# Optimization experiments

Hardware: AMD Instinct MI355X
Metric: run time of the kernel (lower is better)

The kernel has to match this reference:

```python
import jax, jax.numpy as jnp
import numpy as np

B = 4        # samples
GP = 6       # graphs per sample (K*2)
N = 1024     # nodes per graph
DIN = 128    # input feature dim
D = 128      # out_channels
E = 16384    # edges per graph


def setup_inputs() -> dict:
    k = jax.random.split(jax.random.key(0), 10)
    G = B * GP
    s = 0.05
    return {
        "x": jax.random.normal(k[0], (G, N, DIN), jnp.float32),
        "edge_attr": jax.random.uniform(k[1], (G, E, 6), jnp.float32),
        "gcn_W": jax.random.normal(k[2], (4, DIN, D), jnp.float32) * s,
        "gcn_b": jnp.zeros((4, D), jnp.float32),
        "Ws": jax.random.normal(k[3], (4, D, D), jnp.float32) * s,
        "lin1_W": jax.random.normal(k[4], (GP * D, 20), jnp.float32) * s,
        "lin1_b": jnp.zeros((20,), jnp.float32),
        "codefc_W": jax.random.normal(k[5], (20, 2), jnp.float32) * s,
        "codefc_b": jnp.zeros((2,), jnp.float32),
        "lin2_W": jax.random.normal(k[6], (GP * D, GP), jnp.float32) * s,
        "lin2_b": jnp.zeros((GP,), jnp.float32),
        "simfc_W": jax.random.normal(k[7], (GP, 2), jnp.float32) * s,
        "simfc_b": jnp.zeros((2,), jnp.float32),
        "edge_index": jax.random.randint(k[8], (G, 2, E), 0, N, jnp.int64),
    }


def _gcn(x, src, dst, ew, W, b):
    # PyG GCNConv with normalize=True, add_self_loops=True (self-loop weight 1)
    n = x.shape[0]
    deg = jax.ops.segment_sum(ew, dst, num_segments=n) + 1.0
    dinv = jax.lax.rsqrt(deg)
    xw = x @ W
    norm = dinv[src] * ew * dinv[dst]               # [E]
    agg = jax.ops.segment_sum(norm[:, None] * xw[src], dst, num_segments=n)
    return agg + (dinv * dinv)[:, None] * xw + b    # self-loop term + bias


def _gnnlayer(x, ei, ea, gcn_W, gcn_b, Ws):
    # x_tmp = sum_i relu(GCN_i(x, ew=edge_attr[:, i+2])) @ Ws[i]
    src, dst = ei[0], ei[1]
    def chan(W, b, Wmix, ew):
        return jnp.maximum(_gcn(x, src, dst, ew, W, b), 0.0) @ Wmix
    return jax.vmap(chan)(gcn_W, gcn_b, Ws, ea[:, 2:6].T).sum(0)  # [N, D]


def _forward(x, edge_attr, gcn_W, gcn_b, Ws, lin1_W, lin1_b, codefc_W,
             codefc_b, lin2_W, lin2_b, simfc_W, simfc_b, edge_index):
    # per-graph GNN layer over all G = B*GP graphs
    x_tmp = jax.vmap(lambda xg, eig, eag: _gnnlayer(xg, eig, eag, gcn_W, gcn_b, Ws))(
        x, edge_index, edge_attr)                    # [G, N, D]
    g = x_tmp.mean(axis=1).reshape(B, GP * D)        # g_matrix [B, 768]
    # L2-normalize rows (F.normalize eps=1e-12)
    xn = x_tmp / jnp.clip(jnp.linalg.norm(x_tmp, axis=-1, keepdims=True), 1e-12)
    xn = xn.reshape(B, GP, N, D)
    # all-pairs cosine sim -> tanh -> 21-bin histogram on [-1, 1] -> weighted sum
    S = jnp.tanh(jnp.einsum('bind,bjmd->bijnm', xn, xn))   # [B,GP,GP,N,N]
    idx = jnp.clip(jnp.floor((S + 1.0) * (21.0 / 2.0)).astype(jnp.int32), 0, 20)
    centers = jnp.linspace(-1.0, 1.0, 21, dtype=jnp.float32)
    # hist/(N*N) dot centers == mean of per-element bin centers
    sim = centers[idx].mean(axis=(3, 4))             # [B, GP, GP]
    # backnet
    feat = jnp.maximum(g @ lin1_W + lin1_b, 0.0)     # feature_of_G [B, 20]
    code = jax.nn.log_softmax(feat @ codefc_W + codefc_b, axis=1)
    strength = g @ lin2_W + lin2_b                   # [B, GP]
    sim_res = jax.nn.log_softmax((sim.mean(axis=2) * strength) @ simfc_W + simfc_b, axis=1)
    r = 0.4 * code + 0.6 * sim_res
    return r, feat


def reference(x, edge_attr, gcn_W, gcn_b, Ws, lin1_W, lin1_b, codefc_W,
              codefc_b, lin2_W, lin2_b, simfc_W, simfc_b, edge_index):
    return _forward(x, edge_attr, gcn_W, gcn_b, Ws, lin1_W, lin1_b, codefc_W,
                    codefc_b, lin2_W, lin2_b, simfc_W, simfc_b, edge_index)
```

## Files before the change

### kernel.cpp

```cpp
#include <hip/hip_runtime.h>

#define NG 24
#define NB 4
#define GPg 6
#define NN 1024
#define DD 128
#define EE 16384

typedef __bf16 bf16;
typedef __bf16 bf16x8 __attribute__((ext_vector_type(8)));
typedef float f32x4 __attribute__((ext_vector_type(4)));

#define GLOBAL_AS __attribute__((address_space(1)))
#define LDS_AS __attribute__((address_space(3)))

__global__ void k_histw(const int* __restrict__ ei, int* __restrict__ counts,
                        const float* __restrict__ gW, const float* __restrict__ Ws,
                        bf16* __restrict__ gwt, bf16* __restrict__ wst) {
  int bid = blockIdx.x;
  if (bid >= 1536) {
    int i = (bid - 1536) * 256 + threadIdx.x;
    int c = i >> 14, k = (i >> 7) & 127, j = i & 127;
    gwt[(c << 14) | (j << 7) | k] = (bf16)gW[i];
    wst[(j << 9) | (c << 7) | k] = (bf16)Ws[i];
    return;
  }
  int t = bid * 256 + threadIdx.x;
  int g = t >> 14, e = t & (EE - 1);
  int dst = ei[g * 2 * EE + EE + e];
  atomicAdd(&counts[g * NN + dst], 1);
}

__global__ void k_scan(const int* __restrict__ counts, int* __restrict__ offs,
                       int* __restrict__ cursor) {
  __shared__ int sh[NN];
  int g = blockIdx.x, t = threadIdx.x;
  int myc = counts[g * NN + t];
  sh[t] = myc;
  __syncthreads();
  for (int d2 = 1; d2 < NN; d2 <<= 1) {
    int v = (t >= d2) ? sh[t - d2] : 0;
    __syncthreads();
    sh[t] += v;
    __syncthreads();
  }
  int incl = sh[t];
  int excl = incl - myc;
  offs[g * 1025 + t] = excl;
  cursor[g * NN + t] = excl;
  if (t == NN - 1) offs[g * 1025 + NN] = incl;
}

__global__ void k_scatter(const int* __restrict__ ei, const float* __restrict__ ea,
                          int* __restrict__ cursor, int* __restrict__ csrs,
                          float* __restrict__ csre) {
  int t = blockIdx.x * 256 + threadIdx.x;
  if (t >= NG * EE) return;
  int g = t >> 14, e = t & (EE - 1);
  int src = ei[g * 2 * EE + e], dst = ei[g * 2 * EE + EE + e];
  int pos = atomicAdd(&cursor[g * NN + dst], 1);
  size_t idx = (size_t)g * EE + pos;
  csrs[idx] = src;
  const float* p = ea + ((size_t)g * EE + e) * 6;
#pragma unroll
  for (int c = 0; c < 4; c++) csre[idx * 4 + c] = p[2 + c];
}

__global__ void k_deg(const int* __restrict__ offs, const float* __restrict__ csre,
                      float* __restrict__ dinv4) {
  int t = blockIdx.x * 256 + threadIdx.x;
  int c = t & 3, n = (t >> 2) & (NN - 1), g = t >> 12;
  int beg = offs[g * 1025 + n], end = offs[g * 1025 + n + 1];
  const float* ep = csre + (size_t)g * EE * 4 + c;
  float s = 1.0f;
  for (int p = beg; p < end; ++p) s += ep[(size_t)p * 4];
  dinv4[t] = rsqrtf(s);
}

__global__ __launch_bounds__(256) void k_xw(const float* __restrict__ x,
                                            const bf16* __restrict__ gwt,
                                            const float* __restrict__ dinv4,
                                            bf16* __restrict__ xw) {
  int bid = blockIdx.x;
  int gc = bid >> 3, mb = bid & 7;
  int g = gc >> 2, c = gc & 3;
  int lane = threadIdx.x & 63, wid = threadIdx.x >> 6;
  int wm = wid >> 1, wn = wid & 1;
  int row0 = mb * 128 + wm * 64, col0 = wn * 64;
  const float* A = x + (size_t)g * NN * DD;
  const bf16* Bt = gwt + (size_t)c * DD * DD;
  int lr = lane & 15, lk = (lane >> 4) * 8;
  f32x4 acc[4][4] = {};
  for (int kc = 0; kc < 128; kc += 32) {
    bf16x8 a[4], b[4];
#pragma unroll
    for (int i2 = 0; i2 < 4; i2++) {
      const f32x4* pa = (const f32x4*)(A + (size_t)(row0 + i2 * 16 + lr) * DD + kc + lk);
      f32x4 f0 = pa[0], f1 = pa[1];
#pragma unroll
      for (int q = 0; q < 4; q++) { a[i2][q] = (bf16)f0[q]; a[i2][4 + q] = (bf16)f1[q]; }
    }
#pragma unroll
    for (int j2 = 0; j2 < 4; j2++)
      b[j2] = *(const bf16x8*)(Bt + (size_t)(col0 + j2 * 16 + lr) * DD + kc + lk);
#pragma unroll
    for (int i2 = 0; i2 < 4; i2++)
#pragma unroll
      for (int j2 = 0; j2 < 4; j2++)
        acc[i2][j2] = __builtin_amdgcn_mfma_f32_16x16x32_bf16(a[i2], b[j2], acc[i2][j2], 0, 0, 0);
  }
  bf16* out = xw + (size_t)g * NN * 512 + c * 128;
  const float* dv = dinv4 + ((size_t)g * NN) * 4 + c;
  int cr = (lane >> 4) * 4, cc = lane & 15;
#pragma unroll
  for (int i2 = 0; i2 < 4; i2++)
#pragma unroll
    for (int r2 = 0; r2 < 4; r2++) {
      int row = row0 + i2 * 16 + cr + r2;
      float dvv = dv[row * 4];
#pragma unroll
      for (int j2 = 0; j2 < 4; j2++)
        out[(size_t)row * 512 + col0 + j2 * 16 + cc] = (bf16)(acc[i2][j2][r2] * dvv);
    }
}

__global__ __launch_bounds__(256) void k_agg(const int* __restrict__ offs, const int* __restrict__ csrs,
                                             const float* __restrict__ csre, const float* __restrict__ dinv4,
                                             const float* __restrict__ gb, const bf16* __restrict__ xw,
                                             bf16* __restrict__ hb) {
  int bid = blockIdx.x;
  int lb = (bid & 7) * (NG * 256 / 8) + (bid >> 3);
  int g = lb >> 8, n4 = lb & 255;
  int wid = threadIdx.x >> 6, lane = threadIdx.x & 63;
  int n = n4 * 4 + wid;
  int c = lane >> 4, d0 = (lane & 15) * 8;
  const bf16* xwg = xw + (size_t)g * NN * 512;
  int beg = offs[g * 1025 + n], end = offs[g * 1025 + n + 1];
  const int* sp = csrs + (size_t)g * EE;
  const float* ep = csre + (size_t)g * EE * 4;
  float dvn = dinv4[((size_t)g * NN + n) * 4 + c];
  float acc[8] = {};
  int p = beg;
  for (; p + 1 < end; p += 2) {
    int s0 = sp[p], s1 = sp[p + 1];
    float w0 = ep[(size_t)p * 4 + c];
    float w1 = ep[(size_t)(p + 1) * 4 + c];
    bf16x8 v0 = *(const bf16x8*)(xwg + (size_t)s0 * 512 + lane * 8);
    bf16x8 v1 = *(const bf16x8*)(xwg + (size_t)s1 * 512 + lane * 8);
#pragma unroll
    for (int q = 0; q < 8; q++) acc[q] += w0 * (float)v0[q];
#pragma unroll
    for (int q = 0; q < 8; q++) acc[q] += w1 * (float)v1[q];
  }
  if (p < end) {
    int s0 = sp[p];
    float w0 = ep[(size_t)p * 4 + c];
    bf16x8 v0 = *(const bf16x8*)(xwg + (size_t)s0 * 512 + lane * 8);
#pragma unroll
    for (int q = 0; q < 8; q++) acc[q] += w0 * (float)v0[q];
  }
  bf16x8 vs = *(const bf16x8*)(xwg + (size_t)n * 512 + lane * 8);
  bf16x8 o;
#pragma unroll
  for (int q = 0; q < 8; q++) {
    float r2 = dvn * (acc[q] + (float)vs[q]) + gb[c * 128 + d0 + q];
    o[q] = (bf16)fmaxf(r2, 0.f);
  }
  *(bf16x8*)(hb + ((size_t)g * NN + n) * 512 + lane * 8) = o;
}

__global__ __launch_bounds__(256) void k_mixn(const bf16* __restrict__ hb,
                                              const bf16* __restrict__ wst,
                                              float* __restrict__ gmat,
                                              bf16* __restrict__ xn) {
  __shared__ float rowssq[128];
  int bid = blockIdx.x;
  int g = bid >> 3, mb = bid & 7;
  int lane = threadIdx.x & 63, wid = threadIdx.x >> 6;
  int wm = wid >> 1, wn = wid & 1;
  int row0 = mb * 128 + wm * 64, col0 = wn * 64;
  const bf16* H = hb + (size_t)g * NN * 512;
  int lr = lane & 15, lk = (lane >> 4) * 8;
  if (threadIdx.x < 128) rowssq[threadIdx.x] = 0.f;
  f32x4 acc[4][4] = {};
  for (int kc = 0; kc < 512; kc += 32) {
    bf16x8 a[4], b[4];
#pragma unroll
    for (int i2 = 0; i2 < 4; i2++)
      a[i2] = *(const bf16x8*)(H + (size_t)(row0 + i2 * 16 + lr) * 512 + kc + lk);
#pragma unroll
    for (int j2 = 0; j2 < 4; j2++)
      b[j2] = *(const bf16x8*)(wst + (size_t)(col0 + j2 * 16 + lr) * 512 + kc + lk);
#pragma unroll
    for (int i2 = 0; i2 < 4; i2++)
#pragma unroll
      for (int j2 = 0; j2 < 4; j2++)
        acc[i2][j2] = __builtin_amdgcn_mfma_f32_16x16x32_bf16(a[i2], b[j2], acc[i2][j2], 0, 0, 0);
  }
  __syncthreads();
  int cr = (lane >> 4) * 4, cc = lane & 15;
#pragma unroll
  for (int i2 = 0; i2 < 4; i2++)
#pragma unroll
    for (int r2 = 0; r2 < 4; r2++) {
      float s = 0.f;
#pragma unroll
      for (int j2 = 0; j2 < 4; j2++) { float v = acc[i2][j2][r2]; s += v * v; }
#pragma unroll
      for (int d2 = 1; d2 < 16; d2 <<= 1) s += __shfl_xor(s, d2);
      if (cc == 0) atomicAdd(&rowssq[wm * 64 + i2 * 16 + cr + r2], s);
    }
#pragma unroll
  for (int j2 = 0; j2 < 4; j2++) {
    float s = 0.f;
#pragma unroll
    for (int i2 = 0; i2 < 4; i2++)
#pragma unroll
      for (int r2 = 0; r2 < 4; r2++) s += acc[i2][j2][r2];
    s += __shfl_xor(s, 16);
    s += __shfl_xor(s, 32);
    if ((lane >> 4) == 0)
      atomicAdd(&gmat[(g / GPg) * 768 + (g % GPg) * 128 + col0 + j2 * 16 + cc], s * (1.0f / NN));
  }
  __syncthreads();
  bf16* xp = xn + (size_t)g * NN * DD;
#pragma unroll
  for (int i2 = 0; i2 < 4; i2++)
#pragma unroll
    for (int r2 = 0; r2 < 4; r2++) {
      int rowl = wm * 64 + i2 * 16 + cr + r2;
      float inv = 1.0f / fmaxf(sqrtf(rowssq[rowl]), 1e-12f);
#pragma unroll
      for (int j2 = 0; j2 < 4; j2++)
        xp[(size_t)(mb * 128 + rowl) * DD + col0 + j2 * 16 + cc] = (bf16)(acc[i2][j2][r2] * inv);
    }
}

__global__ __launch_bounds__(256, 4) void k_pair(const bf16* __restrict__ xn,
                                                 unsigned* __restrict__ simsum) {
  __shared__ char lds[16384];
  int bid = blockIdx.x;
  int lb = (bid & 7) * 168 + (bid >> 3);
  int b = lb / 336, rem = lb % 336;
  int pj = rem >> 4, rem2 = rem & 15;
  int s128 = rem2 >> 1, half = rem2 & 1;
  int r = pj, i = 0;
  while (r >= 6 - i) { r -= 6 - i; ++i; }
  int j = i + r;
  bool isdiag = (i == j);
  int tb = half * 16, te = tb + 16;
  if (isdiag && 4 * s128 > tb) tb = 4 * s128;
  if (tb >= te) return;
  int lane = threadIdx.x & 63, wid = threadIdx.x >> 6;
  int lr = lane & 15, hi16 = (lane >> 4) * 16;
  const char* Ag = (const char*)(xn + ((size_t)(b * GPg + i) * NN + s128 * 128 + wid * 32) * DD);
  const char* Bg0 = (const char*)(xn + (size_t)(b * GPg + j) * NN * DD);

  bf16x8 a[2][4];
#pragma unroll
  for (int g2 = 0; g2 < 2; g2++)
#pragma unroll
    for (int kc = 0; kc < 4; kc++) {
      a[g2][kc] = *(const bf16x8*)(Ag + (g2 * 16 + lr) * 256 + kc * 64 + hi16);
      asm volatile("" :: "v"(a[g2][kc]));
    }

  auto stage = [&](int buf, int tn) {
    const char* src = Bg0 + tn * 8192;
#pragma unroll
    for (int j2 = 0; j2 < 2; ++j2)
      __builtin_amdgcn_global_load_lds(
          (const GLOBAL_AS void*)(src + (j2 * 16 + lr) * 256 + wid * 64 + hi16),
          (LDS_AS void*)(lds + buf * 8192 + wid * 2048 + j2 * 1024), 16, 0, 0);
  };
  stage(0, tb);
  if (tb + 1 < te) stage(1, tb + 1);

  int cnt = 0;
  int cc = lane & 15, cr = (lane >> 4) * 4;
  for (int t = tb; t < te; ++t) {
    int cur = (t - tb) & 1;
    if (t < te - 1) asm volatile("s_waitcnt vmcnt(2)" ::: "memory");
    else            asm volatile("s_waitcnt vmcnt(0)" ::: "memory");
    __builtin_amdgcn_s_barrier();
    const char* Bl = lds + cur * 8192;
    f32x4 acc[2][2] = {};
#pragma unroll
    for (int kc = 0; kc < 4; kc++) {
      bf16x8 bb[2];
#pragma unroll
      for (int j2 = 0; j2 < 2; j2++)
        bb[j2] = *(const bf16x8*)(Bl + kc * 2048 + j2 * 1024 + lane * 16);
#pragma unroll
      for (int g2 = 0; g2 < 2; g2++)
#pragma unroll
        for (int j2 = 0; j2 < 2; j2++)
          acc[g2][j2] = __builtin_amdgcn_mfma_f32_16x16x32_bf16(a[g2][kc], bb[j2], acc[g2][j2], 0, 0, 0);
    }
    asm volatile("s_waitcnt lgkmcnt(0)" ::: "memory");
    __builtin_amdgcn_sched_barrier(0);
    __builtin_amdgcn_s_barrier();
    if (t + 2 < te) stage(cur, t + 2);
    if (isdiag && t < 4 * s128 + 4) {
      int tc = 0;
#pragma unroll
      for (int g2 = 0; g2 < 2; g2++)
#pragma unroll
        for (int j2 = 0; j2 < 2; j2++)
#pragma unroll
          for (int r2 = 0; r2 < 4; r2++) {
            float v = acc[g2][j2][r2];
            float e = __builtin_amdgcn_exp2f(v * 2.8853900817779268f);
            int idx = (int)(21.f - 21.f * __builtin_amdgcn_rcpf(e + 1.f));
            int lm = t * 32 + j2 * 16 + cc;
            int ln = s128 * 128 + wid * 32 + g2 * 16 + cr + r2;
            tc += (lm > ln) ? 2 * idx : (lm == ln ? idx : 0);
          }
      cnt += tc;
    } else {
      int tc = 0;
#pragma unroll
      for (int g2 = 0; g2 < 2; g2++)
#pragma unroll
        for (int j2 = 0; j2 < 2; j2++)
#pragma unroll
          for (int r2 = 0; r2 < 4; r2++) {
            float v = acc[g2][j2][r2];
            float e = __builtin_amdgcn_exp2f(v * 2.8853900817779268f);
            tc += (int)(21.f - 21.f * __builtin_amdgcn_rcpf(e + 1.f));
          }
      cnt += isdiag ? 2 * tc : tc;
    }
  }
#pragma unroll
  for (int d2 = 32; d2; d2 >>= 1) cnt += __shfl_xor(cnt, d2);
  if (lane == 0) atomicAdd(&simsum[((size_t)b * GPg + i) * GPg + j], (unsigned)cnt);
}

__global__ void k_back(const float* __restrict__ gmat, const unsigned* __restrict__ simsum,
                       const float* __restrict__ l1W, const float* __restrict__ l1b,
                       const float* __restrict__ cfW, const float* __restrict__ cfb,
                       const float* __restrict__ l2W, const float* __restrict__ l2b,
                       const float* __restrict__ sfW, const float* __restrict__ sfb,
                       float* __restrict__ out) {
  __shared__ float feat[NB][20];
  __shared__ float strength[NB][GPg];
  __shared__ float simmean[NB][GPg];
  int t = threadIdx.x, g = t >> 3, l = t & 7;
  if (g < 80) {
    int b = g / 20, jj = g % 20;
    float s = 0.f;
#pragma unroll 8
    for (int k = l; k < 768; k += 8) s += gmat[b * 768 + k] * l1W[k * 20 + jj];
    s += __shfl_xor(s, 1); s += __shfl_xor(s, 2); s += __shfl_xor(s, 4);
    if (l == 0) {
      float f = fmaxf(s + l1b[jj], 0.f);
      feat[b][jj] = f;
      out[8 + b * 20 + jj] = f;
    }
  } else if (g < 104) {
    int q = g - 80, b = q / GPg, pp = q % GPg;
    float s = 0.f;
#pragma unroll 8
    for (int k = l; k < 768; k += 8) s += gmat[b * 768 + k] * l2W[k * GPg + pp];
    s += __shfl_xor(s, 1); s += __shfl_xor(s, 2); s += __shfl_xor(s, 4);
    if (l == 0) strength[b][pp] = s + l2b[pp];
  } else if (t >= 832 && t < 856) {
    int q = t - 832; int b = q / GPg, ii = q % GPg;
    float s = 0.f;
    for (int jj = 0; jj < GPg; jj++) {
      int lo = ii < jj ? ii : jj, hi = ii < jj ? jj : ii;
      s += -1.0f + 0.1f * (float)simsum[(b * GPg + lo) * GPg + hi] * (1.0f / (1024.f * 1024.f));
    }
    simmean[b][ii] = s * (1.0f / GPg);
  }
  __syncthreads();
  if (t < NB) {
    int b = t;
    float l1v[2], l2v[2];
#pragma unroll
    for (int u = 0; u < 2; u++) {
      float s = cfb[u];
      for (int jj = 0; jj < 20; jj++) s += feat[b][jj] * cfW[jj * 2 + u];
      l1v[u] = s;
      float s2 = sfb[u];
      for (int pp = 0; pp < GPg; pp++) s2 += simmean[b][pp] * strength[b][pp] * sfW[pp * 2 + u];
      l2v[u] = s2;
    }
    float m1 = fmaxf(l1v[0], l1v[1]);
    float lse1 = m1 + logf(expf(l1v[0] - m1) + expf(l1v[1] - m1));
    float m2 = fmaxf(l2v[0], l2v[1]);
    float lse2 = m2 + logf(expf(l2v[0] - m2) + expf(l2v[1] - m2));
    out[b * 2 + 0] = 0.4f * (l1v[0] - lse1) + 0.6f * (l2v[0] - lse2);
    out[b * 2 + 1] = 0.4f * (l1v[1] - lse1) + 0.6f * (l2v[1] - lse2);
  }
}

extern "C" void kernel_launch(void* const* d_in, const int* in_sizes, int n_in,
                              void* d_out, int out_size, void* d_ws, size_t ws_size,
                              hipStream_t stream) {
  const float* x   = (const float*)d_in[0];
  const float* ea  = (const float*)d_in[1];
  const float* gW  = (const float*)d_in[2];
  const float* gb  = (const float*)d_in[3];
  const float* Ws  = (const float*)d_in[4];
  const float* l1W = (const float*)d_in[5];
  const float* l1b = (const float*)d_in[6];
  const float* cfW = (const float*)d_in[7];
  const float* cfb = (const float*)d_in[8];
  const float* l2W = (const float*)d_in[9];
  const float* l2b = (const float*)d_in[10];
  const float* sfW = (const float*)d_in[11];
  const float* sfb = (const float*)d_in[12];
  const int* eidx  = (const int*)d_in[13];
  float* out = (float*)d_out;

  char* w = (char*)d_ws;
  auto alloc = [&](size_t bytes) { char* p = w; w += (bytes + 255) & ~(size_t)255; return (void*)p; };
  bf16* gwt     = (bf16*)alloc(4 * DD * DD * 2);
  bf16* wst     = (bf16*)alloc(4 * DD * DD * 2);
  int* counts   = (int*)alloc((size_t)NG * NN * 4);
  float* dinv4  = (float*)alloc((size_t)NG * NN * 4 * 4);
  int* offs     = (int*)alloc((size_t)NG * 1025 * 4);
  int* cursor   = (int*)alloc((size_t)NG * NN * 4);
  int* csrs     = (int*)alloc((size_t)NG * EE * 4);
  float* csre   = (float*)alloc((size_t)NG * EE * 4 * 4);
  bf16* xw      = (bf16*)alloc((size_t)NG * NN * 512 * 2);
  bf16* hb      = (bf16*)alloc((size_t)NG * NN * 512 * 2);
  float* gmat   = (float*)alloc((size_t)NB * 768 * 4);
  unsigned* simsum = (unsigned*)alloc((size_t)NB * 36 * 4);
  bf16* xn      = (bf16*)alloc((size_t)NG * NN * DD * 2);

  hipMemsetAsync(counts, 0, (size_t)NG * NN * 4, stream);
  hipMemsetAsync(gmat, 0, 12288 + 576, stream);

  k_histw<<<1792, 256, 0, stream>>>(eidx, counts, gW, Ws, gwt, wst);
  k_scan<<<NG, 1024, 0, stream>>>(counts, offs, cursor);
  k_scatter<<<(NG * EE) / 256, 256, 0, stream>>>(eidx, ea, cursor, csrs, csre);
  k_deg<<<(NG * NN * 4) / 256, 256, 0, stream>>>(offs, csre, dinv4);
  k_xw<<<NG * 4 * 8, 256, 0, stream>>>(x, gwt, dinv4, xw);
  k_agg<<<NG * 256, 256, 0, stream>>>(offs, csrs, csre, dinv4, gb, xw, hb);
  k_mixn<<<NG * 8, 256, 0, stream>>>(hb, wst, gmat, xn);
  k_pair<<<1344, 256, 0, stream>>>(xn, simsum);
  k_back<<<1, 1024, 0, stream>>>(gmat, simsum, l1W, l1b, cfW, cfb, l2W, l2b, sfW, sfb, out);
}
```

Before: 185.3 us.

## Restructure pair kernel to keep B tile resident in LDS and stream A rows

The all-pairs similarity kernel now loads one 64-row B tile into LDS once per block and has each wave stream 32-row A strips from global memory, replacing the previous double-buffered B streaming with a fixed A strip in registers. This removes the per-iteration barriers and waitcnt pipelining, and widens each wave's MFMA tile to 2x4. Diagonal blocks now bound the A loop so fewer tiles are computed, and zero counts skip the atomic. The CSR scatter also uses vectorized float2 loads and a single 16-byte store for the edge weights. The cost is that A loads are no longer prefetched, so global latency is exposed inside the loop, and occupancy launch bounds were relaxed.

```diff
diff --git a/kernel.cpp b/kernel.cpp
--- a/kernel.cpp
+++ b/kernel.cpp
@@ -62,8 +62,10 @@
   size_t idx = (size_t)g * EE + pos;
   csrs[idx] = src;
   const float* p = ea + ((size_t)g * EE + e) * 6;
-#pragma unroll
-  for (int c = 0; c < 4; c++) csre[idx * 4 + c] = p[2 + c];
+  float2 q0 = *(const float2*)(p + 2);
+  float2 q1 = *(const float2*)(p + 4);
+  f32x4 v; v[0] = q0.x; v[1] = q0.y; v[2] = q1.x; v[3] = q1.y;
+  *(f32x4*)(csre + idx * 4) = v;
 }
 
 __global__ void k_deg(const int* __restrict__ offs, const float* __restrict__ csre,
@@ -236,84 +238,66 @@
     }
 }
 
-__global__ __launch_bounds__(256, 4) void k_pair(const bf16* __restrict__ xn,
-                                                 unsigned* __restrict__ simsum) {
+__global__ __launch_bounds__(256) void k_pair(const bf16* __restrict__ xn,
+                                              unsigned* __restrict__ simsum) {
   __shared__ char lds[16384];
   int bid = blockIdx.x;
   int lb = (bid & 7) * 168 + (bid >> 3);
   int b = lb / 336, rem = lb % 336;
-  int pj = rem >> 4, rem2 = rem & 15;
-  int s128 = rem2 >> 1, half = rem2 & 1;
+  int pj = rem >> 4, c16 = rem & 15;
   int r = pj, i = 0;
   while (r >= 6 - i) { r -= 6 - i; ++i; }
   int j = i + r;
   bool isdiag = (i == j);
-  int tb = half * 16, te = tb + 16;
-  if (isdiag && 4 * s128 > tb) tb = 4 * s128;
-  if (tb >= te) return;
   int lane = threadIdx.x & 63, wid = threadIdx.x >> 6;
   int lr = lane & 15, hi16 = (lane >> 4) * 16;
-  const char* Ag = (const char*)(xn + ((size_t)(b * GPg + i) * NN + s128 * 128 + wid * 32) * DD);
-  const char* Bg0 = (const char*)(xn + (size_t)(b * GPg + j) * NN * DD);
-
-  bf16x8 a[2][4];
-#pragma unroll
-  for (int g2 = 0; g2 < 2; g2++)
+  const char* Ag0 = (const char*)(xn + (size_t)(b * GPg + i) * NN * DD);
+  const char* Bg  = (const char*)(xn + (size_t)(b * GPg + j) * NN * DD) + c16 * 16384;
+
+#pragma unroll
+  for (int j2 = 0; j2 < 4; ++j2)
+    __builtin_amdgcn_global_load_lds(
+        (const GLOBAL_AS void*)(Bg + (j2 * 16 + lr) * 256 + wid * 64 + hi16),
+        (LDS_AS void*)(lds + wid * 4096 + j2 * 1024 + lane * 16), 16, 0, 0);
+  __syncthreads();
+
+  int smax = isdiag ? 2 * c16 + 2 : 32;
+  int cnt = 0;
+  int cc = lr, cr = (lane >> 4) * 4;
+  for (int s = wid; s < smax; s += 4) {
+    const char* Ag = Ag0 + s * 8192;
+    bf16x8 a[2][4];
+#pragma unroll
+    for (int g2 = 0; g2 < 2; g2++)
+#pragma unroll
+      for (int kc = 0; kc < 4; kc++)
+        a[g2][kc] = *(const bf16x8*)(Ag + (g2 * 16 + lr) * 256 + kc * 64 + hi16);
+    f32x4 acc[2][4] = {};
 #pragma unroll
     for (int kc = 0; kc < 4; kc++) {
-      a[g2][kc] = *(const bf16x8*)(Ag + (g2 * 16 + lr) * 256 + kc * 64 + hi16);
-      asm volatile("" :: "v"(a[g2][kc]));
-    }
-
-  auto stage = [&](int buf, int tn) {
-    const char* src = Bg0 + tn * 8192;
-#pragma unroll
-    for (int j2 = 0; j2 < 2; ++j2)
-      __builtin_amdgcn_global_load_lds(
-          (const GLOBAL_AS void*)(src + (j2 * 16 + lr) * 256 + wid * 64 + hi16),
-          (LDS_AS void*)(lds + buf * 8192 + wid * 2048 + j2 * 1024), 16, 0, 0);
-  };
-  stage(0, tb);
-  if (tb + 1 < te) stage(1, tb + 1);
-
-  int cnt = 0;
-  int cc = lane & 15, cr = (lane >> 4) * 4;
-  for (int t = tb; t < te; ++t) {
-    int cur = (t - tb) & 1;
-    if (t < te - 1) asm volatile("s_waitcnt vmcnt(2)" ::: "memory");
-    else            asm volatile("s_waitcnt vmcnt(0)" ::: "memory");
-    __builtin_amdgcn_s_barrier();
-    const char* Bl = lds + cur * 8192;
-    f32x4 acc[2][2] = {};
-#pragma unroll
-    for (int kc = 0; kc < 4; kc++) {
-      bf16x8 bb[2];
-#pragma unroll
-      for (int j2 = 0; j2 < 2; j2++)
-        bb[j2] = *(const bf16x8*)(Bl + kc * 2048 + j2 * 1024 + lane * 16);
+      bf16x8 bb[4];
+#pragma unroll
+      for (int j2 = 0; j2 < 4; j2++)
+        bb[j2] = *(const bf16x8*)(lds + kc * 4096 + j2 * 1024 + lane * 16);
 #pragma unroll
       for (int g2 = 0; g2 < 2; g2++)
 #pragma unroll
-        for (int j2 = 0; j2 < 2; j2++)
+        for (int j2 = 0; j2 < 4; j2++)
           acc[g2][j2] = __builtin_amdgcn_mfma_f32_16x16x32_bf16(a[g2][kc], bb[j2], acc[g2][j2], 0, 0, 0);
     }
-    asm volatile("s_waitcnt lgkmcnt(0)" ::: "memory");
-    __builtin_amdgcn_sched_barrier(0);
-    __builtin_amdgcn_s_barrier();
-    if (t + 2 < te) stage(cur, t + 2);
-    if (isdiag && t < 4 * s128 + 4) {
+    if (isdiag && s >= 2 * c16) {
       int tc = 0;
 #pragma unroll
       for (int g2 = 0; g2 < 2; g2++)
 #pragma unroll
-        for (int j2 = 0; j2 < 2; j2++)
+        for (int j2 = 0; j2 < 4; j2++)
 #pragma unroll
           for (int r2 = 0; r2 < 4; r2++) {
             float v = acc[g2][j2][r2];
             float e = __builtin_amdgcn_exp2f(v * 2.8853900817779268f);
             int idx = (int)(21.f - 21.f * __builtin_amdgcn_rcpf(e + 1.f));
-            int lm = t * 32 + j2 * 16 + cc;
-            int ln = s128 * 128 + wid * 32 + g2 * 16 + cr + r2;
+            int lm = c16 * 64 + j2 * 16 + cc;
+            int ln = s * 32 + g2 * 16 + cr + r2;
             tc += (lm > ln) ? 2 * idx : (lm == ln ? idx : 0);
           }
       cnt += tc;
@@ -322,7 +306,7 @@
 #pragma unroll
       for (int g2 = 0; g2 < 2; g2++)
 #pragma unroll
-        for (int j2 = 0; j2 < 2; j2++)
+        for (int j2 = 0; j2 < 4; j2++)
 #pragma unroll
           for (int r2 = 0; r2 < 4; r2++) {
             float v = acc[g2][j2][r2];
@@ -334,7 +318,7 @@
   }
 #pragma unroll
   for (int d2 = 32; d2; d2 >>= 1) cnt += __shfl_xor(cnt, d2);
-  if (lane == 0) atomicAdd(&simsum[((size_t)b * GPg + i) * GPg + j], (unsigned)cnt);
+  if (lane == 0 && cnt != 0) atomicAdd(&simsum[((size_t)b * GPg + i) * GPg + j], (unsigned)cnt);
 }
 
 __global__ void k_back(const float* __restrict__ gmat, const unsigned* __restrict__ simsum,
```

Result: slower. 196.6 us (+6.1%).
